# Performance work log

Hardware: AMD Instinct MI355X
Metric: run time of the kernel (lower is better)

## Reference

```python
import jax, jax.numpy as jnp
import numpy as np

H = 32          # num query heads
KV = 8          # num kv heads
D = 64          # head_dim
WIN = 512       # sliding_window
BASE = 10000.0  # rope base


def setup_inputs() -> dict:
    key = jax.random.key(0)
    ks = jax.random.split(key, 5)
    B, S, DIM = 2, 2048, 2048
    x = jax.random.normal(ks[0], (B, S, DIM), dtype=jnp.float32)
    wq = jax.random.normal(ks[1], (H * D, DIM), dtype=jnp.float32) * 0.02
    wk = jax.random.normal(ks[2], (KV * D, DIM), dtype=jnp.float32) * 0.02
    wv = jax.random.normal(ks[3], (KV * D, DIM), dtype=jnp.float32) * 0.02
    wo = jax.random.normal(ks[4], (DIM, H * D), dtype=jnp.float32) * 0.02
    return {"x": x, "wq": wq, "wk": wk, "wv": wv, "wo": wo}


def _rope_tables(S):
    inv_freq = 1.0 / (BASE ** (jnp.arange(0, D, 2, dtype=jnp.float32) / D))
    t = jnp.arange(S, dtype=jnp.float32)
    freqs = t[:, None] * inv_freq[None, :]          # [S, D/2]
    emb = jnp.concatenate([freqs, freqs], axis=-1)  # [S, D]
    return jnp.cos(emb)[:, None, :], jnp.sin(emb)[:, None, :]  # [S,1,D]


def _rotate_half(u):
    return jnp.concatenate([-u[..., D // 2:], u[..., :D // 2]], axis=-1)


def reference(x, wq, wk, wv, wo):
    B, S, _ = x.shape
    q = (x @ wq.T).reshape(B, S, H, D)
    k = (x @ wk.T).reshape(B, S, KV, D)
    v = (x @ wv.T).reshape(B, S, KV, D)

    cos, sin = _rope_tables(S)  # [S,1,D] broadcasts over batch and heads
    q = q * cos + _rotate_half(q) * sin
    k = k * cos + _rotate_half(k) * sin

    q = q.transpose(0, 2, 1, 3)                        # [B,H,S,D]
    k = jnp.repeat(k.transpose(0, 2, 1, 3), H // KV, axis=1)  # [B,H,S,D]
    v = jnp.repeat(v.transpose(0, 2, 1, 3), H // KV, axis=1)

    scale = 1.0 / jnp.sqrt(jnp.float32(D))
    scores = jnp.einsum('bhqd,bhkd->bhqk', q, k) * scale  # [B,H,S,S]

    i = jnp.arange(S)[:, None]
    j = jnp.arange(S)[None, :]
    window_mask = jnp.abs(i - j) > WIN // 2   # True = masked (outside window)
    causal_mask = j > i                        # True = masked (future)
    masked = window_mask | causal_mask
    scores = jnp.where(masked[None, None], -jnp.inf, scores)

    attn = jax.nn.softmax(scores, axis=-1)
    out = jnp.einsum('bhqk,bhkd->bhqd', attn, v)  # [B,H,S,D]
    out = out.transpose(0, 2, 1, 3).reshape(B, S, H * D)
    return out @ wo.T
```

## Files before the change

### kernel.cpp

```cpp
#include <hip/hip_runtime.h>
#include <cstdint>
#include <cstddef>

#define SLEN 2048
#define NB 2
#define NH 32
#define NKV 8
#define HD 64
#define MROWS 4096
#define QDIM 2048
#define KVDIM 512
#define WINH 256

typedef float f32x4 __attribute__((ext_vector_type(4)));
typedef __bf16 bf16x8 __attribute__((ext_vector_type(8)));

__device__ __forceinline__ unsigned short f2bf(float f) {
  union { float f; unsigned u; } v; v.f = f;
  unsigned r = v.u + 0x7fffu + ((v.u >> 16) & 1u);
  return (unsigned short)(r >> 16);
}
__device__ __forceinline__ float bf2f(unsigned short h) {
  union { unsigned u; float f; } v; v.u = ((unsigned)h) << 16;
  return v.f;
}
__device__ __forceinline__ unsigned pk2(float a, float b) {
  return (unsigned)f2bf(a) | ((unsigned)f2bf(b) << 16);
}
__device__ __forceinline__ unsigned cvtpk(float a, float b) {
  unsigned r;
  asm("v_cvt_pk_bf16_f32 %0, %1, %2" : "=v"(r) : "v"(a), "v"(b));
  return r;
}
__device__ __forceinline__ uint4 cvt16(float4 a, float4 b) {
  uint4 u;
  u.x = pk2(a.x, a.y); u.y = pk2(a.z, a.w);
  u.z = pk2(b.x, b.y); u.w = pk2(b.z, b.w);
  return u;
}
__device__ __forceinline__ void async16(const unsigned short* g, unsigned short* l) {
  __builtin_amdgcn_global_load_lds(
      (const __attribute__((address_space(1))) unsigned int*)g,
      (__attribute__((address_space(3))) unsigned int*)l, 16, 0, 0);
}

__global__ void rope_table(float2* __restrict__ tab) {
  int tid = blockIdx.x * 256 + threadIdx.x;
  int d = tid & 31;
  int s = tid >> 5;
  float inv = expf((float)d * (-2.0f / 64.0f) * 9.210340371976184f);
  float ang = (float)s * inv;
  float sn, cs;
  sincosf(ang, &sn, &cs);
  tab[tid] = make_float2(cs, sn);
}

__global__ void conv_bf16(const float* __restrict__ src, unsigned short* __restrict__ dst) {
  size_t t = (size_t)blockIdx.x * 256 + threadIdx.x;
  float4 a = *(const float4*)(src + t * 8);
  float4 b = *(const float4*)(src + t * 8 + 4);
  *(uint4*)(dst + t * 8) = cvt16(a, b);
}

__global__ void conv_wqkv(const float* __restrict__ wq, const float* __restrict__ wk,
                          const float* __restrict__ wv, unsigned short* __restrict__ dst) {
  size_t t = (size_t)blockIdx.x * 256 + threadIdx.x;
  size_t e = t * 8;
  int row = (int)(e >> 11);
  const float* src; size_t off;
  if (row < 2048)       { src = wq; off = e; }
  else if (row < 2560)  { src = wk; off = e - (size_t)2048 * 2048; }
  else                  { src = wv; off = e - (size_t)2560 * 2048; }
  float4 a = *(const float4*)(src + off);
  float4 b = *(const float4*)(src + off + 4);
  *(uint4*)(dst + e) = cvt16(a, b);
}

__global__ void rope_qk(unsigned short* __restrict__ qb,
                        unsigned short* __restrict__ kb,
                        const float* __restrict__ tabf) {
  const float2* tab = (const float2*)tabf;
  int tid = blockIdx.x * 256 + threadIdx.x;
  int oct = tid & 3;
  int head = (tid >> 2) % 40;
  int row = tid / 160;
  int s = row & (SLEN - 1);
  int d0 = oct * 8;
  unsigned short* p = (head < NH)
      ? qb + (size_t)row * QDIM + head * HD
      : kb + (size_t)row * KVDIM + (head - NH) * HD;
  uint4 u0 = *(const uint4*)(p + d0);
  uint4 u1 = *(const uint4*)(p + d0 + 32);
  const unsigned short* a16 = (const unsigned short*)&u0;
  const unsigned short* b16 = (const unsigned short*)&u1;
  unsigned short o0[8], o1[8];
#pragma unroll
  for (int j = 0; j < 8; ++j) {
    float2 cs = tab[s * 32 + d0 + j];
    float a = bf2f(a16[j]), b = bf2f(b16[j]);
    o0[j] = f2bf(a * cs.x - b * cs.y);
    o1[j] = f2bf(b * cs.x + a * cs.y);
  }
  *(uint4*)(p + d0)      = *(const uint4*)o0;
  *(uint4*)(p + d0 + 32) = *(const uint4*)o1;
}

__global__ __launch_bounds__(512, 2) void qkv_gemm(
    const unsigned short* __restrict__ Ap, const unsigned short* __restrict__ Bp,
    unsigned short* __restrict__ o_q, unsigned short* __restrict__ o_k,
    unsigned short* __restrict__ o_v)
{
  extern __shared__ unsigned short L[];
  constexpr int NT = 32;

  const int bid = blockIdx.x;
  const int swz = (bid & 7) * 32 + (bid >> 3);
  const int bm0 = (swz & 15) * 256;
  const int bn0 = (swz >> 4) * 192;

  const int tid = threadIdx.x;
  const int lane = tid & 63, wid = tid >> 6;
  const int g = lane >> 4, cl = lane & 15;
  const int wm = wid >> 2, wn = wid & 3;

  const int r0 = wid * 32 + (lane >> 2);
  const int s0 = (((lane & 3) ^ ((lane >> 3) & 3)) << 3);
  const unsigned short* gA = Ap + (size_t)(bm0 + r0) * 2048 + s0;
  const unsigned short* gB = Bp + (size_t)(bn0 + r0) * 2048 + s0;

  const int slotus = ((g ^ ((cl >> 1) & 3)) << 3);
  const int aread = (wm * 128 + cl) * 32 + slotus;
  const int bread = (wn * 48 + cl) * 32 + slotus;

#define REG_(b, op, kh) ((((b) * 2 + (op)) * 2 + (kh)) * 8192)
#define STG(op, kh, tt, db) do { \
    const unsigned short* s_ = ((op) ? gB : gA) + (tt) * 64 + (kh) * 32; \
    unsigned short* d_ = L + REG_(db, op, kh) + wid * 1024; \
    async16(s_, d_); \
    async16(s_ + 16 * 2048, d_ + 512); \
  } while (0)
#define LDA(dst, kh, mh) \
    _Pragma("unroll") for (int mf = 0; mf < 4; ++mf) \
      dst[mf] = *(const bf16x8*)&L[REG_(cb, 0, kh) + aread + (mh) * 2048 + mf * 512];
#define LDB(dst, kh) \
    _Pragma("unroll") for (int nf = 0; nf < 3; ++nf) \
      dst[nf] = *(const bf16x8*)&L[REG_(cb, 1, kh) + bread + nf * 512];
#define MM(mh, A, B) do { \
    __builtin_amdgcn_s_setprio(1); \
    _Pragma("unroll") for (int mf = 0; mf < 4; ++mf) \
      _Pragma("unroll") for (int nf = 0; nf < 3; ++nf) \
        acc[(mh) * 4 + mf][nf] = __builtin_amdgcn_mfma_f32_16x16x32_bf16( \
            A[mf], B[nf], acc[(mh) * 4 + mf][nf], 0, 0, 0); \
    __builtin_amdgcn_s_setprio(0); \
  } while (0)

  f32x4 acc[8][3] = {};

  STG(0, 0, 0, 0); STG(1, 0, 0, 0); STG(0, 1, 0, 0); STG(1, 1, 0, 0);
  STG(0, 0, 1, 1); STG(1, 0, 1, 1);
  asm volatile("s_waitcnt vmcnt(4)" ::: "memory");
  __builtin_amdgcn_s_barrier();
  __builtin_amdgcn_sched_barrier(0);

#pragma unroll 1
  for (int t = 0; t < NT; ++t) {
    const int cb = t & 1, nb = cb ^ 1;
    bf16x8 a00[4], a10[4], a01[4], a11[4], b0[3], b1[3];

    if (t + 1 < NT) STG(0, 1, t + 1, nb);
    LDA(a00, 0, 0); LDB(b0, 0);
    if (t + 1 < NT) STG(1, 1, t + 1, nb);
    LDA(a10, 0, 1);
    MM(0, a00, b0);
    LDA(a01, 1, 0); LDB(b1, 1);
    MM(1, a10, b0);
    asm volatile("s_waitcnt lgkmcnt(0)" ::: "memory");
    __builtin_amdgcn_s_barrier();
    __builtin_amdgcn_sched_barrier(0);
    if (t + 2 < NT) STG(0, 0, t + 2, cb);
    LDA(a11, 1, 1);
    MM(0, a01, b1);
    if (t + 2 < NT) STG(1, 0, t + 2, cb);
    MM(1, a11, b1);
    if (t + 2 < NT) { asm volatile("s_waitcnt vmcnt(4)" ::: "memory"); }
    else            { asm volatile("s_waitcnt vmcnt(0)" ::: "memory"); }
    asm volatile("s_waitcnt lgkmcnt(0)" ::: "memory");
    __builtin_amdgcn_s_barrier();
    __builtin_amdgcn_sched_barrier(0);
  }
#undef MM
#undef LDB
#undef LDA
#undef STG
#undef REG_

  const int rb = bm0 + wm * 128;
#pragma unroll
  for (int m = 0; m < 8; ++m)
#pragma unroll
    for (int nf = 0; nf < 3; ++nf) {
      const int col = bn0 + wn * 48 + nf * 16 + cl;
      if (col < QDIM) {
#pragma unroll
        for (int p = 0; p < 4; ++p) {
          int row = rb + m * 16 + g * 4 + p;
          o_q[(size_t)row * QDIM + col] = f2bf(acc[m][nf][p]);
        }
      } else if (col < QDIM + KVDIM) {
#pragma unroll
        for (int p = 0; p < 4; ++p) {
          int row = rb + m * 16 + g * 4 + p;
          o_k[(size_t)row * KVDIM + col - QDIM] = f2bf(acc[m][nf][p]);
        }
      } else {
        int vc = col - QDIM - KVDIM;
        int kvh = vc >> 6, d = vc & 63;
        int row0 = rb + m * 16 + g * 4;
        int bb = row0 >> 11, s = row0 & (SLEN - 1);
        unsigned short* dst = o_v + (((size_t)(bb * NKV + kvh) * HD + d) << 11) + s;
        uint2 u;
        u.x = pk2(acc[m][nf][0], acc[m][nf][1]);
        u.y = pk2(acc[m][nf][2], acc[m][nf][3]);
        *(uint2*)dst = u;
      }
    }
}

__global__ __launch_bounds__(512, 2) void out_gemm(
    const unsigned short* __restrict__ Ap, const unsigned short* __restrict__ Bp,
    float* __restrict__ o_f)
{
  extern __shared__ unsigned short L[];
  constexpr int NT = 32;

  const int bid = blockIdx.x;
  const int swz = (bid & 7) * 32 + (bid >> 3);
  const int bm0 = (swz & 31) * 128;
  const int bn0 = (swz >> 5) * 256;

  const int tid = threadIdx.x;
  const int lane = tid & 63, wid = tid >> 6;
  const int g = lane >> 4, cl = lane & 15;
  const int wm = wid >> 2, wn = wid & 3;

  const int s0 = (((lane & 3) ^ ((lane >> 3) & 3)) << 3);
  const unsigned short* gA = Ap + (size_t)(bm0 + wid * 16 + (lane >> 2)) * 2048 + s0;
  const unsigned short* gB = Bp + (size_t)(bn0 + wid * 32 + (lane >> 2)) * 2048 + s0;

  const int slotus = ((g ^ ((cl >> 1) & 3)) << 3);
  const int aread = (wm * 64 + cl) * 32 + slotus;
  const int bread = (wn * 64 + cl) * 32 + slotus;

#define REGA_(b, kh) ((b) * 24576 + (kh) * 4096)
#define REGB_(b, kh) ((b) * 24576 + 8192 + (kh) * 8192)
#define STGA(kh, tt, db) \
    async16(gA + (tt) * 64 + (kh) * 32, L + REGA_(db, kh) + wid * 512)
#define STGB(kh, tt, db) do { \
    const unsigned short* s_ = gB + (tt) * 64 + (kh) * 32; \
    unsigned short* d_ = L + REGB_(db, kh) + wid * 1024; \
    async16(s_, d_); \
    async16(s_ + 16 * 2048, d_ + 512); \
  } while (0)
#define LA(dst, kh, mp) \
    _Pragma("unroll") for (int mf = 0; mf < 2; ++mf) \
      dst[mf] = *(const bf16x8*)&L[REGA_(cb, kh) + aread + (mp) * 1024 + mf * 512];
#define LB(dst, kh) \
    _Pragma("unroll") for (int nf = 0; nf < 4; ++nf) \
      dst[nf] = *(const bf16x8*)&L[REGB_(cb, kh) + bread + nf * 512];
#define MMO(mp, A, B) do { \
    __builtin_amdgcn_s_setprio(1); \
    _Pragma("unroll") for (int mf = 0; mf < 2; ++mf) \
      _Pragma("unroll") for (int nf = 0; nf < 4; ++nf) \
        acc[(mp) * 2 + mf][nf] = __builtin_amdgcn_mfma_f32_16x16x32_bf16( \
            A[mf], B[nf], acc[(mp) * 2 + mf][nf], 0, 0, 0); \
    __builtin_amdgcn_s_setprio(0); \
  } while (0)

  f32x4 acc[4][4] = {};

  STGA(0, 0, 0); STGB(0, 0, 0); STGA(1, 0, 0); STGB(1, 0, 0);
  STGA(0, 1, 1); STGB(0, 1, 1);
  asm volatile("s_waitcnt vmcnt(3)" ::: "memory");
  __builtin_amdgcn_s_barrier();
  __builtin_amdgcn_sched_barrier(0);

#pragma unroll 1
  for (int t = 0; t < NT; ++t) {
    const int cb = t & 1, nb = cb ^ 1;
    bf16x8 p00[2], p10[2], p01[2], p11[2], b0[4], b1[4];

    if (t + 1 < NT) STGA(1, t + 1, nb);
    LA(p00, 0, 0); LB(b0, 0);
    if (t + 1 < NT) STGB(1, t + 1, nb);
    LA(p10, 0, 1);
    MMO(0, p00, b0);
    LA(p01, 1, 0); LB(b1, 1);
    MMO(1, p10, b0);
    asm volatile("s_waitcnt lgkmcnt(0)" ::: "memory");
    __builtin_amdgcn_s_barrier();
    __builtin_amdgcn_sched_barrier(0);
    if (t + 2 < NT) STGA(0, t + 2, cb);
    LA(p11, 1, 1);
    MMO(0, p01, b1);
    if (t + 2 < NT) STGB(0, t + 2, cb);
    MMO(1, p11, b1);
    if (t + 2 < NT) { asm volatile("s_waitcnt vmcnt(3)" ::: "memory"); }
    else            { asm volatile("s_waitcnt vmcnt(0)" ::: "memory"); }
    asm volatile("s_waitcnt lgkmcnt(0)" ::: "memory");
    __builtin_amdgcn_s_barrier();
    __builtin_amdgcn_sched_barrier(0);
  }
#undef MMO
#undef LB
#undef LA
#undef STGB
#undef STGA
#undef REGB_
#undef REGA_

  const int rb = bm0 + wm * 64;
  const int colb = bn0 + wn * 64;
#pragma unroll
  for (int m = 0; m < 4; ++m)
#pragma unroll
    for (int nf = 0; nf < 4; ++nf)
#pragma unroll
      for (int p = 0; p < 4; ++p) {
        int row = rb + m * 16 + g * 4 + p;
        o_f[(size_t)row * 2048 + colb + nf * 16 + cl] = acc[m][nf][p];
      }
}

__global__ __launch_bounds__(256) void attn(
    const unsigned short* __restrict__ qb, const unsigned short* __restrict__ kb,
    const unsigned short* __restrict__ vt, unsigned short* __restrict__ ao)
{
  __shared__ __align__(16) unsigned short Plds[4][2][16][40];
  const int lane = threadIdx.x & 63, wid = threadIdx.x >> 6;
  const int g = lane >> 4, cl = lane & 15;
  const int qt = blockIdx.x * 4 + wid;
  const int bh = qt >> 6, tl = qt & 63;
  const int i0 = tl * 32;
  const int b = bh >> 5, h = bh & 31, kvh = (bh & 31) >> 2;
  const int qi0 = i0 + cl, qi1 = i0 + 16 + cl;

  const unsigned short* qp0 = qb + ((size_t)(b * SLEN + qi0) * NH + h) * HD + g * 8;
  const unsigned short* qp1 = qb + ((size_t)(b * SLEN + qi1) * NH + h) * HD + g * 8;
  bf16x8 qf00 = *(const bf16x8*)qp0, qf01 = *(const bf16x8*)(qp0 + 32);
  bf16x8 qf10 = *(const bf16x8*)qp1, qf11 = *(const bf16x8*)(qp1 + 32);

  const unsigned short* kbase = kb + ((size_t)b * SLEN * NKV + kvh) * HD + g * 8;
  const unsigned short* vbase = vt + ((size_t)(b * NKV + kvh) * HD) * SLEN;

  f32x4 acc0[4] = {}, acc1[4] = {};
  float m0 = -1e30f, l0 = 0.f, m1 = -1e30f, l1 = 0.f;
  const int jb = (i0 > WINH) ? (i0 - WINH) : 0;

#define LOADK(dst, jj) do { \
    _Pragma("unroll") for (int t = 0; t < 2; ++t) { \
      int krow = (jj) + 16 * t + cl; \
      if (krow > SLEN - 1) krow = SLEN - 1; \
      const unsigned short* kp_ = kbase + (size_t)krow * KVDIM; \
      dst[t * 2]     = *(const bf16x8*)kp_; \
      dst[t * 2 + 1] = *(const bf16x8*)(kp_ + 32); \
    } \
  } while (0)

#define SOFTMAX(SAC, MR, LR, ACC, QI, QF) do { \
    float sm[2][4]; float mx = -1e30f; \
    _Pragma("unroll") for (int t = 0; t < 2; ++t) \
      _Pragma("unroll") for (int p = 0; p < 4; ++p) { \
        int kj = j0 + 16 * t + 4 * g + p; \
        bool ok = (kj <= (QI)) && ((QI) - kj <= WINH); \
        float v = ok ? SAC[t][p] * 0.125f : -1e30f; \
        sm[t][p] = v; mx = fmaxf(mx, v); \
      } \
    mx = fmaxf(mx, __shfl_xor(mx, 16)); \
    mx = fmaxf(mx, __shfl_xor(mx, 32)); \
    float mnew = fmaxf(MR, mx); \
    float corr = __expf(MR - mnew); \
    float ps = 0.f; unsigned pw00, pw01, pw10, pw11; \
    { \
      float p0 = __expf(sm[0][0] - mnew), p1 = __expf(sm[0][1] - mnew); \
      float p2 = __expf(sm[0][2] - mnew), p3 = __expf(sm[0][3] - mnew); \
      ps += p0 + p1 + p2 + p3; pw00 = cvtpk(p0, p1); pw01 = cvtpk(p2, p3); \
      float p4 = __expf(sm[1][0] - mnew), p5 = __expf(sm[1][1] - mnew); \
      float p6 = __expf(sm[1][2] - mnew), p7 = __expf(sm[1][3] - mnew); \
      ps += p4 + p5 + p6 + p7; pw10 = cvtpk(p4, p5); pw11 = cvtpk(p6, p7); \
    } \
    ps += __shfl_xor(ps, 16); ps += __shfl_xor(ps, 32); \
    LR = LR * corr + ps; MR = mnew; \
    _Pragma("unroll") for (int vb2 = 0; vb2 < 4; ++vb2) \
      _Pragma("unroll") for (int p = 0; p < 4; ++p) ACC[vb2][p] *= corr; \
    *(unsigned*)&Plds[wid][QF][cl][4 * g]          = pw00; \
    *(unsigned*)&Plds[wid][QF][cl][4 * g + 2]      = pw01; \
    *(unsigned*)&Plds[wid][QF][cl][16 + 4 * g]     = pw10; \
    *(unsigned*)&Plds[wid][QF][cl][16 + 4 * g + 2] = pw11; \
  } while (0)

#define BODY(CUR, NXT) do { \
    LOADK(NXT, j0 + 32);                          \
    bf16x8 vf[4]; \
    { \
      int jv = j0 + g * 8; \
      if (jv > SLEN - 8) jv = SLEN - 8; \
      _Pragma("unroll") for (int vb2 = 0; vb2 < 4; ++vb2) \
        vf[vb2] = *(const bf16x8*)(vbase + (size_t)(vb2 * 16 + cl) * SLEN + jv); \
    } \
    f32x4 s0[2], s1[2]; \
    _Pragma("unroll") for (int t = 0; t < 2; ++t) { \
      f32x4 z = {}; \
      z = __builtin_amdgcn_mfma_f32_16x16x32_bf16(CUR[t * 2], qf00, z, 0, 0, 0); \
      z = __builtin_amdgcn_mfma_f32_16x16x32_bf16(CUR[t * 2 + 1], qf01, z, 0, 0, 0); \
      s0[t] = z; \
      f32x4 z2 = {}; \
      z2 = __builtin_amdgcn_mfma_f32_16x16x32_bf16(CUR[t * 2], qf10, z2, 0, 0, 0); \
      z2 = __builtin_amdgcn_mfma_f32_16x16x32_bf16(CUR[t * 2 + 1], qf11, z2, 0, 0, 0); \
      s1[t] = z2; \
    } \
    SOFTMAX(s0, m0, l0, acc0, qi0, 0); \
    SOFTMAX(s1, m1, l1, acc1, qi1, 1); \
    bf16x8 pf0 = *(const bf16x8*)&Plds[wid][0][cl][g * 8]; \
    bf16x8 pf1 = *(const bf16x8*)&Plds[wid][1][cl][g * 8]; \
    _Pragma("unroll") for (int vb2 = 0; vb2 < 4; ++vb2) \
      acc0[vb2] = __builtin_amdgcn_mfma_f32_16x16x32_bf16(vf[vb2], pf0, acc0[vb2], 0, 0, 0); \
    _Pragma("unroll") for (int vb2 = 0; vb2 < 4; ++vb2) \
      acc1[vb2] = __builtin_amdgcn_mfma_f32_16x16x32_bf16(vf[vb2], pf1, acc1[vb2], 0, 0, 0); \
  } while (0)

  bf16x8 kA[4], kB[4];
  LOADK(kA, jb);
  int j0 = jb;
  for (;;) {
    BODY(kA, kB); j0 += 32; if (j0 > i0) break;
    BODY(kB, kA); j0 += 32; if (j0 > i0) break;
  }
#undef BODY
#undef SOFTMAX
#undef LOADK

  float inv0 = 1.0f / l0, inv1 = 1.0f / l1;
  unsigned short* op0 = ao + ((size_t)(b * SLEN + qi0) * NH + h) * HD;
  unsigned short* op1 = ao + ((size_t)(b * SLEN + qi1) * NH + h) * HD;
#pragma unroll
  for (int vbk = 0; vbk < 4; ++vbk) {
    *(unsigned*)(op0 + vbk * 16 + g * 4)     = cvtpk(acc0[vbk][0] * inv0, acc0[vbk][1] * inv0);
    *(unsigned*)(op0 + vbk * 16 + g * 4 + 2) = cvtpk(acc0[vbk][2] * inv0, acc0[vbk][3] * inv0);
    *(unsigned*)(op1 + vbk * 16 + g * 4)     = cvtpk(acc1[vbk][0] * inv1, acc1[vbk][1] * inv1);
    *(unsigned*)(op1 + vbk * 16 + g * 4 + 2) = cvtpk(acc1[vbk][2] * inv1, acc1[vbk][3] * inv1);
  }
}

extern "C" void kernel_launch(void* const* d_in, const int* in_sizes, int n_in,
                              void* d_out, int out_size, void* d_ws, size_t ws_size,
                              hipStream_t stream) {
  const float* x  = (const float*)d_in[0];
  const float* wq = (const float*)d_in[1];
  const float* wk = (const float*)d_in[2];
  const float* wv = (const float*)d_in[3];
  const float* wo = (const float*)d_in[4];
  float* out = (float*)d_out;

  char* w = (char*)d_ws;
  unsigned short* wqkvb = (unsigned short*)w; w += (size_t)3136 * 2048 * 2;
  unsigned short* xb    = (unsigned short*)w; w += (size_t)MROWS * QDIM * 2;
  unsigned short* qb    = (unsigned short*)w; w += (size_t)MROWS * QDIM * 2;
  unsigned short* kb    = (unsigned short*)w; w += (size_t)MROWS * KVDIM * 2;
  unsigned short* vt    = (unsigned short*)w; w += (size_t)MROWS * KVDIM * 2;
  float* tab            = (float*)w;          w += (size_t)SLEN * 32 * 8;
  unsigned short* wob = wqkvb;
  unsigned short* ao  = xb;

  hipFuncSetAttribute((const void*)qkv_gemm,
                      hipFuncAttributeMaxDynamicSharedMemorySize, 131072);
  hipFuncSetAttribute((const void*)out_gemm,
                      hipFuncAttributeMaxDynamicSharedMemorySize, 98304);

  rope_table<<<SLEN * 32 / 256, 256, 0, stream>>>((float2*)tab);
  conv_bf16<<<(MROWS * 2048) / (8 * 256), 256, 0, stream>>>(x, xb);
  conv_wqkv<<<(3072 * 2048) / (8 * 256), 256, 0, stream>>>(wq, wk, wv, wqkvb);
  qkv_gemm<<<256, 512, 131072, stream>>>(xb, wqkvb, qb, kb, vt);
  rope_qk<<<(MROWS * 40 * 4) / 256, 256, 0, stream>>>(qb, kb, tab);
  conv_bf16<<<(2048 * 2048) / (8 * 256), 256, 0, stream>>>(wo, wob);
  attn<<<(NB * NH * (SLEN / 32)) / 4, 256, 0, stream>>>(qb, kb, vt, ao);
  out_gemm<<<256, 512, 98304, stream>>>(ao, wob, out);
}
```

Before: 168.8 us.

## Fuse RoPE into QKV GEMM epilogue, merge conversions, prefetch V in attention

Applies rotary embedding inside the QKV GEMM epilogue. Accumulators are staged through shared memory so each lane can read its rotate-half partner column, which removes the separate rope_qk kernel and its read-modify-write of Q/K. The x and weight fp32-to-bf16 conversions are merged into one launch. The attention kernel now double-buffers V fragments alongside K. The cost is two block barriers per m-iteration in the epilogue, a non-unrolled store loop, more registers in attention, and RoPE now being applied to fp32 accumulators before rounding instead of after.

```diff
diff --git a/kernel.cpp b/kernel.cpp
--- a/kernel.cpp
+++ b/kernel.cpp
@@ -55,6 +55,29 @@
   tab[tid] = make_float2(cs, sn);
 }
 
+__global__ void conv_xw(const float* __restrict__ x,
+                        const float* __restrict__ wq, const float* __restrict__ wk,
+                        const float* __restrict__ wv,
+                        unsigned short* __restrict__ xb, unsigned short* __restrict__ wqkvb) {
+  size_t t = (size_t)blockIdx.x * 256 + threadIdx.x;
+  if (t < (size_t)1048576) {
+    size_t e = t * 8;
+    float4 a = *(const float4*)(x + e);
+    float4 b = *(const float4*)(x + e + 4);
+    *(uint4*)(xb + e) = cvt16(a, b);
+  } else {
+    size_t e = (t - 1048576) * 8;
+    int row = (int)(e >> 11);
+    const float* src; size_t off;
+    if (row < 2048)       { src = wq; off = e; }
+    else if (row < 2560)  { src = wk; off = e - (size_t)2048 * 2048; }
+    else                  { src = wv; off = e - (size_t)2560 * 2048; }
+    float4 a = *(const float4*)(src + off);
+    float4 b = *(const float4*)(src + off + 4);
+    *(uint4*)(wqkvb + e) = cvt16(a, b);
+  }
+}
+
 __global__ void conv_bf16(const float* __restrict__ src, unsigned short* __restrict__ dst) {
   size_t t = (size_t)blockIdx.x * 256 + threadIdx.x;
   float4 a = *(const float4*)(src + t * 8);
@@ -62,51 +85,9 @@
   *(uint4*)(dst + t * 8) = cvt16(a, b);
 }
 
-__global__ void conv_wqkv(const float* __restrict__ wq, const float* __restrict__ wk,
-                          const float* __restrict__ wv, unsigned short* __restrict__ dst) {
-  size_t t = (size_t)blockIdx.x * 256 + threadIdx.x;
-  size_t e = t * 8;
-  int row = (int)(e >> 11);
-  const float* src; size_t off;
-  if (row < 2048)       { src = wq; off = e; }
-  else if (row < 2560)  { src = wk; off = e - (size_t)2048 * 2048; }
-  else                  { src = wv; off = e - (size_t)2560 * 2048; }
-  float4 a = *(const float4*)(src + off);
-  float4 b = *(const float4*)(src + off + 4);
-  *(uint4*)(dst + e) = cvt16(a, b);
-}
-
-__global__ void rope_qk(unsigned short* __restrict__ qb,
-                        unsigned short* __restrict__ kb,
-                        const float* __restrict__ tabf) {
-  const float2* tab = (const float2*)tabf;
-  int tid = blockIdx.x * 256 + threadIdx.x;
-  int oct = tid & 3;
-  int head = (tid >> 2) % 40;
-  int row = tid / 160;
-  int s = row & (SLEN - 1);
-  int d0 = oct * 8;
-  unsigned short* p = (head < NH)
-      ? qb + (size_t)row * QDIM + head * HD
-      : kb + (size_t)row * KVDIM + (head - NH) * HD;
-  uint4 u0 = *(const uint4*)(p + d0);
-  uint4 u1 = *(const uint4*)(p + d0 + 32);
-  const unsigned short* a16 = (const unsigned short*)&u0;
-  const unsigned short* b16 = (const unsigned short*)&u1;
-  unsigned short o0[8], o1[8];
-#pragma unroll
-  for (int j = 0; j < 8; ++j) {
-    float2 cs = tab[s * 32 + d0 + j];
-    float a = bf2f(a16[j]), b = bf2f(b16[j]);
-    o0[j] = f2bf(a * cs.x - b * cs.y);
-    o1[j] = f2bf(b * cs.x + a * cs.y);
-  }
-  *(uint4*)(p + d0)      = *(const uint4*)o0;
-  *(uint4*)(p + d0 + 32) = *(const uint4*)o1;
-}
-
 __global__ __launch_bounds__(512, 2) void qkv_gemm(
     const unsigned short* __restrict__ Ap, const unsigned short* __restrict__ Bp,
+    const float* __restrict__ tabf,
     unsigned short* __restrict__ o_q, unsigned short* __restrict__ o_k,
     unsigned short* __restrict__ o_v)
 {
@@ -194,25 +175,16 @@
 #undef STG
 #undef REG_
 
+  float* E = (float*)L;
+  const float2* tab = (const float2*)tabf;
   const int rb = bm0 + wm * 128;
-#pragma unroll
-  for (int m = 0; m < 8; ++m)
+#pragma unroll 1
+  for (int m = 0; m < 8; ++m) {
 #pragma unroll
     for (int nf = 0; nf < 3; ++nf) {
-      const int col = bn0 + wn * 48 + nf * 16 + cl;
-      if (col < QDIM) {
-#pragma unroll
-        for (int p = 0; p < 4; ++p) {
-          int row = rb + m * 16 + g * 4 + p;
-          o_q[(size_t)row * QDIM + col] = f2bf(acc[m][nf][p]);
-        }
-      } else if (col < QDIM + KVDIM) {
-#pragma unroll
-        for (int p = 0; p < 4; ++p) {
-          int row = rb + m * 16 + g * 4 + p;
-          o_k[(size_t)row * KVDIM + col - QDIM] = f2bf(acc[m][nf][p]);
-        }
-      } else {
+      const int bc = wn * 48 + nf * 16 + cl;
+      const int col = bn0 + bc;
+      if (col >= QDIM + KVDIM) {
         int vc = col - QDIM - KVDIM;
         int kvh = vc >> 6, d = vc & 63;
         int row0 = rb + m * 16 + g * 4;
@@ -222,8 +194,35 @@
         u.x = pk2(acc[m][nf][0], acc[m][nf][1]);
         u.y = pk2(acc[m][nf][2], acc[m][nf][3]);
         *(uint2*)dst = u;
+      } else {
+#pragma unroll
+        for (int p = 0; p < 4; ++p)
+          E[(wm * 16 + g * 4 + p) * 200 + bc] = acc[m][nf][p];
       }
     }
+    __syncthreads();
+#pragma unroll
+    for (int nf = 0; nf < 3; ++nf) {
+      const int bc = wn * 48 + nf * 16 + cl;
+      const int col = bn0 + bc;
+      if (col < QDIM + KVDIM) {
+        const int dh = col & 63;
+        const int d31 = dh & 31;
+#pragma unroll
+        for (int p = 0; p < 4; ++p) {
+          int row = rb + m * 16 + g * 4 + p;
+          int s = row & (SLEN - 1);
+          float2 cs = tab[s * 32 + d31];
+          float a = acc[m][nf][p];
+          float pv = E[(wm * 16 + g * 4 + p) * 200 + (bc ^ 32)];
+          float r = (dh & 32) ? (a * cs.x + pv * cs.y) : (a * cs.x - pv * cs.y);
+          if (col < QDIM) o_q[(size_t)row * QDIM + col] = f2bf(r);
+          else            o_k[(size_t)row * KVDIM + col - QDIM] = f2bf(r);
+        }
+      }
+    }
+    __syncthreads();
+  }
 }
 
 __global__ __launch_bounds__(512, 2) void out_gemm(
@@ -364,6 +363,13 @@
       dst[t * 2]     = *(const bf16x8*)kp_; \
       dst[t * 2 + 1] = *(const bf16x8*)(kp_ + 32); \
     } \
+  } while (0)
+
+#define LOADV(dst, jj) do { \
+    int jv = (jj) + g * 8; \
+    if (jv > SLEN - 8) jv = SLEN - 8; \
+    _Pragma("unroll") for (int vb2 = 0; vb2 < 4; ++vb2) \
+      dst[vb2] = *(const bf16x8*)(vbase + (size_t)(vb2 * 16 + cl) * SLEN + jv); \
   } while (0)
 
 #define SOFTMAX(SAC, MR, LR, ACC, QI, QF) do { \
@@ -398,24 +404,18 @@
     *(unsigned*)&Plds[wid][QF][cl][16 + 4 * g + 2] = pw11; \
   } while (0)
 
-#define BODY(CUR, NXT) do { \
-    LOADK(NXT, j0 + 32);                          \
-    bf16x8 vf[4]; \
-    { \
-      int jv = j0 + g * 8; \
-      if (jv > SLEN - 8) jv = SLEN - 8; \
-      _Pragma("unroll") for (int vb2 = 0; vb2 < 4; ++vb2) \
-        vf[vb2] = *(const bf16x8*)(vbase + (size_t)(vb2 * 16 + cl) * SLEN + jv); \
-    } \
+#define BODY(KC, KN, VC, VN) do { \
+    LOADK(KN, j0 + 32);                           \
+    LOADV(VN, j0 + 32);                           \
     f32x4 s0[2], s1[2]; \
     _Pragma("unroll") for (int t = 0; t < 2; ++t) { \
       f32x4 z = {}; \
-      z = __builtin_amdgcn_mfma_f32_16x16x32_bf16(CUR[t * 2], qf00, z, 0, 0, 0); \
-      z = __builtin_amdgcn_mfma_f32_16x16x32_bf16(CUR[t * 2 + 1], qf01, z, 0, 0, 0); \
+      z = __builtin_amdgcn_mfma_f32_16x16x32_bf16(KC[t * 2], qf00, z, 0, 0, 0); \
+      z = __builtin_amdgcn_mfma_f32_16x16x32_bf16(KC[t * 2 + 1], qf01, z, 0, 0, 0); \
       s0[t] = z; \
       f32x4 z2 = {}; \
-      z2 = __builtin_amdgcn_mfma_f32_16x16x32_bf16(CUR[t * 2], qf10, z2, 0, 0, 0); \
-      z2 = __builtin_amdgcn_mfma_f32_16x16x32_bf16(CUR[t * 2 + 1], qf11, z2, 0, 0, 0); \
+      z2 = __builtin_amdgcn_mfma_f32_16x16x32_bf16(KC[t * 2], qf10, z2, 0, 0, 0); \
+      z2 = __builtin_amdgcn_mfma_f32_16x16x32_bf16(KC[t * 2 + 1], qf11, z2, 0, 0, 0); \
       s1[t] = z2; \
     } \
     SOFTMAX(s0, m0, l0, acc0, qi0, 0); \
@@ -423,20 +423,21 @@
     bf16x8 pf0 = *(const bf16x8*)&Plds[wid][0][cl][g * 8]; \
     bf16x8 pf1 = *(const bf16x8*)&Plds[wid][1][cl][g * 8]; \
     _Pragma("unroll") for (int vb2 = 0; vb2 < 4; ++vb2) \
-      acc0[vb2] = __builtin_amdgcn_mfma_f32_16x16x32_bf16(vf[vb2], pf0, acc0[vb2], 0, 0, 0); \
+      acc0[vb2] = __builtin_amdgcn_mfma_f32_16x16x32_bf16(VC[vb2], pf0, acc0[vb2], 0, 0, 0); \
     _Pragma("unroll") for (int vb2 = 0; vb2 < 4; ++vb2) \
-      acc1[vb2] = __builtin_amdgcn_mfma_f32_16x16x32_bf16(vf[vb2], pf1, acc1[vb2], 0, 0, 0); \
-  } while (0)
-
-  bf16x8 kA[4], kB[4];
-  LOADK(kA, jb);
+      acc1[vb2] = __builtin_amdgcn_mfma_f32_16x16x32_bf16(VC[vb2], pf1, acc1[vb2], 0, 0, 0); \
+  } while (0)
+
+  bf16x8 kA[4], kB[4], vA[4], vB[4];
+  LOADK(kA, jb); LOADV(vA, jb);
   int j0 = jb;
   for (;;) {
-    BODY(kA, kB); j0 += 32; if (j0 > i0) break;
-    BODY(kB, kA); j0 += 32; if (j0 > i0) break;
+    BODY(kA, kB, vA, vB); j0 += 32; if (j0 > i0) break;
+    BODY(kB, kA, vB, vA); j0 += 32; if (j0 > i0) break;
   }
 #undef BODY
 #undef SOFTMAX
+#undef LOADV
 #undef LOADK
 
   float inv0 = 1.0f / l0, inv1 = 1.0f / l1;
@@ -477,10 +478,8 @@
                       hipFuncAttributeMaxDynamicSharedMemorySize, 98304);
 
   rope_table<<<SLEN * 32 / 256, 256, 0, stream>>>((float2*)tab);
-  conv_bf16<<<(MROWS * 2048) / (8 * 256), 256, 0, stream>>>(x, xb);
-  conv_wqkv<<<(3072 * 2048) / (8 * 256), 256, 0, stream>>>(wq, wk, wv, wqkvb);
-  qkv_gemm<<<256, 512, 131072, stream>>>(xb, wqkvb, qb, kb, vt);
-  rope_qk<<<(MROWS * 40 * 4) / 256, 256, 0, stream>>>(qb, kb, tab);
+  conv_xw<<<7168, 256, 0, stream>>>(x, wq, wk, wv, xb, wqkvb);
+  qkv_gemm<<<256, 512, 131072, stream>>>(xb, wqkvb, tab, qb, kb, vt);
   conv_bf16<<<(2048 * 2048) / (8 * 256), 256, 0, stream>>>(wo, wob);
   attn<<<(NB * NH * (SLEN / 32)) / 4, 256, 0, stream>>>(qb, kb, vt, ao);
   out_gemm<<<256, 512, 98304, stream>>>(ao, wob, out);
```

Result: slower. 201.3 us (+19.2%).
